# Optimization experiments

Measured on AMD Instinct MI355X. Metric: run time of the kernel, lower is better.

## Reference

```python
import jax, jax.numpy as jnp
import numpy as np

N_WIRES = 12
DEPTH = 4
IN_DIM = 256
BATCH = 4096


def _apply_rx(state, theta, wire, n):
    """Apply RX(theta) = [[cos(t/2), -i sin(t/2)], [-i sin(t/2), cos(t/2)]] on `wire`.
    state: (batch, 2^n) complex. theta: scalar or (batch,) float."""
    half = theta * 0.5
    c = jnp.reshape(jnp.cos(half), (-1, 1, 1))  # broadcasts for scalar or per-batch
    s = jnp.reshape(jnp.sin(half), (-1, 1, 1))
    L, R = 2 ** wire, 2 ** (n - wire - 1)
    st = state.reshape(-1, L, 2, R)
    a0, a1 = st[:, :, 0], st[:, :, 1]
    b0 = c * a0 - 1j * s * a1
    b1 = -1j * s * a0 + c * a1
    return jnp.stack([b0, b1], axis=2).reshape(state.shape)


def _apply_cnot_adj(state, ctrl, n):
    """CNOT with control=ctrl, target=ctrl+1 (adjacent wires)."""
    L, R = 2 ** ctrl, 2 ** (n - ctrl - 2)
    st = state.reshape(-1, L, 2, 2, R)
    c0 = st[:, :, 0]
    c1 = st[:, :, 1, ::-1]  # flip target bit when control=1
    return jnp.stack([c0, c1], axis=2).reshape(state.shape)


def _pauli_z_signs(n):
    idx = np.arange(2 ** n)
    # wire 0 is the most-significant bit (torchquantum convention)
    bits = (idx[:, None] >> (n - 1 - np.arange(n))[None, :]) & 1
    return (1.0 - 2.0 * bits).astype(np.float32)  # (2^n, n)


def setup_inputs() -> dict:
    key = jax.random.key(0)
    k1, k2, k3 = jax.random.split(key, 3)
    x = jax.random.normal(k1, (BATCH, IN_DIM), dtype=jnp.float32)
    W = jax.random.normal(k2, (N_WIRES, IN_DIM), dtype=jnp.float32)
    params = jax.random.normal(k3, (DEPTH, N_WIRES, 1), dtype=jnp.float32)
    return {"x": x, "W": W, "params": params}


def reference(x, W, params):
    n = W.shape[0]
    depth = params.shape[0]
    batch = x.shape[0]
    angles = x @ W.T  # (batch, n) -- nn.Linear without bias
    state = jnp.zeros((batch, 2 ** n), dtype=jnp.complex64).at[:, 0].set(1.0)
    # data-encoding RX layer (per-batch angles)
    for w in range(n):
        state = _apply_rx(state, angles[:, w], w, n)
    # variational layers: RX(params) then CNOT ladder
    for d in range(depth):
        for w in range(n):
            state = _apply_rx(state, params[d, w, 0], w, n)
        for w in range(n - 1):
            state = _apply_cnot_adj(state, w, n)
    probs = jnp.real(state * jnp.conj(state))  # (batch, 2^n)
    signs = jnp.asarray(_pauli_z_signs(n))     # (2^n, n)
    return probs @ signs  # <Z_w> per wire, (batch, n)
```

## Files before the change

### kernel.cpp

```cpp
#include <hip/hip_runtime.h>
#include <math.h>

#define N_WIRES 12
#define DEPTH   4
#define NGATES  (DEPTH * N_WIRES)
#define IN_DIM  256
#define ROWS_PER_BLOCK 16
#define XSTRIDE 272
#define K_BLOCKS 16


struct ConstTab {
    unsigned m[NGATES];
    float    wt[N_WIRES][NGATES];
    unsigned sh[N_WIRES][3];
};
struct MeasTab {
    unsigned S[N_WIRES];
};

__global__ __launch_bounds__(256)
void consts_kernel(const float* __restrict__ params, float* __restrict__ ws,
                   ConstTab ct)
{
    __shared__ float acc[N_WIRES * 16];
    const int t = threadIdx.x;
    if (t < N_WIRES * 16) acc[t] = 0.f;
    __syncthreads();

    const unsigned k = blockIdx.x * 256u + (unsigned)t;

    float th[NGATES];
    #pragma unroll
    for (int g = 0; g < NGATES; ++g) th[g] = params[g];

    float P[N_WIRES];
    #pragma unroll
    for (int w = 0; w < N_WIRES; ++w) P[w] = 0.f;

    #pragma unroll
    for (int g = 0; g < NGATES; ++g) {
        unsigned par = (unsigned)(__popc(ct.m[g] & k) & 1);
        float sg = __int_as_float(__float_as_int(th[g]) ^ (int)(par << 31));
        #pragma unroll
        for (int w = 0; w < N_WIRES; ++w)
            P[w] = fmaf(sg, ct.wt[w][g], P[w]);
    }

    #pragma unroll
    for (int w = 0; w < N_WIRES; ++w) {
        float sn, cs;
        sincosf(P[w], &sn, &cs);
        unsigned kap =  ((k >> ct.sh[w][0]) & 1u)
                     | (((k >> ct.sh[w][1]) & 1u) << 1)
                     | (((k >> ct.sh[w][2]) & 1u) << 2);
        atomicAdd(&acc[w * 16 + kap], cs);
        atomicAdd(&acc[w * 16 + 8 + kap], sn);
    }
    __syncthreads();
    if (t < N_WIRES * 16)
        ws[blockIdx.x * (N_WIRES * 16) + t] = acc[t];
}

__global__ __launch_bounds__(256)
void batch_kernel(const float* __restrict__ x, const float* __restrict__ W,
                  const float* __restrict__ ws, float* __restrict__ out,
                  MeasTab mt)
{
    __shared__ float xl[ROWS_PER_BLOCK * XSTRIDE];
    __shared__ float wl[N_WIRES * IN_DIM];
    __shared__ float al[ROWS_PER_BLOCK * N_WIRES];
    __shared__ float cl[N_WIRES * 16];
    const int t = threadIdx.x;
    const int rowbase = blockIdx.x * ROWS_PER_BLOCK;

    const float4* x4 = (const float4*)(x + (size_t)rowbase * IN_DIM);
    #pragma unroll
    for (int j = 0; j < 4; ++j) {
        int f   = t + 256 * j;
        int row = f >> 6;
        int c4  = f & 63;
        float4 v = x4[f];
        *(float4*)&xl[row * XSTRIDE + c4 * 4] = v;
    }
    const float4* W4 = (const float4*)W;
    #pragma unroll
    for (int j = 0; j < 3; ++j) {
        int f = t + 256 * j;
        ((float4*)wl)[f] = W4[f];
    }
    if (t < N_WIRES * 16) {
        float v = 0.f;
        #pragma unroll
        for (int p = 0; p < K_BLOCKS; ++p) v += ws[p * (N_WIRES * 16) + t];
        cl[t] = v;
    }
    __syncthreads();

    const int r = t >> 4, p = t & 15;
    float partial[N_WIRES];
    #pragma unroll
    for (int w = 0; w < N_WIRES; ++w) partial[w] = 0.f;
    for (int i = 0; i < 16; ++i) {
        float xv = xl[r * XSTRIDE + i * 16 + p];
        #pragma unroll
        for (int w = 0; w < N_WIRES; ++w)
            partial[w] = fmaf(xv, wl[w * IN_DIM + i * 16 + p], partial[w]);
    }
    #pragma unroll
    for (int w = 0; w < N_WIRES; ++w) {
        float v = partial[w];
        v += __shfl_xor(v, 1, 16);
        v += __shfl_xor(v, 2, 16);
        v += __shfl_xor(v, 4, 16);
        v += __shfl_xor(v, 8, 16);
        partial[w] = v;
    }
    if (p < N_WIRES) al[r * N_WIRES + p] = partial[p];
    __syncthreads();

    if (t < ROWS_PER_BLOCK * N_WIRES) {
        const int r2 = t / N_WIRES;
        const int w  = t - r2 * N_WIRES;
        unsigned S = mt.S[w];
        int pos[3], nb = 0;
        for (int b = 0; b < N_WIRES; ++b) if ((S >> b) & 1) pos[nb++] = b;
        float a[3] = {0.f, 0.f, 0.f};
        for (int j = 0; j < nb; ++j) a[j] = al[r2 * N_WIRES + pos[j]];
        float o = 0.f;
        const int nk = 1 << nb;
        for (int kap = 0; kap < nk; ++kap) {
            float B = 0.f;
            for (int j = 0; j < nb; ++j)
                B += ((kap >> j) & 1) ? -a[j] : a[j];
            float sn, cs;
            __sincosf(B, &sn, &cs);
            o = fmaf(cs,  cl[w * 16 + kap],     o);
            o = fmaf(-sn, cl[w * 16 + 8 + kap], o);
        }
        out[(size_t)(rowbase + r2) * N_WIRES + w] = o * (1.f / 4096.f);
    }
}

static void gf2_mul(const unsigned* A, const unsigned* B, unsigned* C) {
    for (int i = 0; i < N_WIRES; ++i) {
        unsigned r = 0;
        for (int v = 0; v < N_WIRES; ++v)
            if ((A[i] >> v) & 1) r ^= B[v];
        C[i] = r;
    }
}
static int popc_host(unsigned v) { int c = 0; while (v) { c += v & 1; v >>= 1; } return c; }

extern "C" void kernel_launch(void* const* d_in, const int* in_sizes, int n_in,
                              void* d_out, int out_size, void* d_ws, size_t ws_size,
                              hipStream_t stream) {
    const float* x      = (const float*)d_in[0];
    const float* W      = (const float*)d_in[1];
    const float* params = (const float*)d_in[2];
    float* out          = (float*)d_out;
    float* wsf          = (float*)d_ws;

    unsigned L[N_WIRES], Linv[N_WIRES];
    for (int w = 0; w < N_WIRES; ++w) {
        L[w]    = (1u << (w + 1)) - 1u;
        Linv[w] = (w == 0) ? 1u : ((1u << w) | (1u << (w - 1)));
    }
    unsigned Mp[DEPTH + 1][N_WIRES], Mi[DEPTH + 1][N_WIRES];
    for (int w = 0; w < N_WIRES; ++w) { Mp[0][w] = 1u << w; Mi[0][w] = 1u << w; }
    for (int d = 1; d <= DEPTH; ++d) {
        gf2_mul(L, Mp[d - 1], Mp[d]);
        gf2_mul(Linv, Mi[d - 1], Mi[d]);
    }

    ConstTab ct;
    MeasTab  mt;
    for (int d = 0; d < DEPTH; ++d)
        for (int w = 0; w < N_WIRES; ++w) {
            unsigned m = 0;
            for (int u = 0; u < N_WIRES; ++u)
                if ((Mi[d][u] >> w) & 1) m |= (1u << u);
            ct.m[d * N_WIRES + w] = m;
        }
    for (int w = 0; w < N_WIRES; ++w) mt.S[w] = Mp[DEPTH][w];

    for (int w = 0; w < N_WIRES; ++w) {
        for (int g = 0; g < NGATES; ++g)
            ct.wt[w][g] = (popc_host(ct.m[g] & mt.S[w]) & 1) ? 1.f : 0.f;
        int nb = 0;
        for (int b = 0; b < N_WIRES; ++b)
            if ((mt.S[w] >> b) & 1) ct.sh[w][nb++] = (unsigned)b;
        for (; nb < 3; ++nb) ct.sh[w][nb] = 31u;
    }

    const int batch = in_sizes[0] / IN_DIM;

    hipLaunchKernelGGL(consts_kernel, dim3(K_BLOCKS), dim3(256), 0, stream,
                       params, wsf, ct);
    hipLaunchKernelGGL(batch_kernel, dim3(batch / ROWS_PER_BLOCK), dim3(256), 0, stream,
                       x, W, wsf, out, mt);
}
```

Baseline: 75.39 us.

## Fuse constant-table kernel into batch kernel with compile-time GF(2) tables

Removes the separate consts kernel and its workspace round-trip. Each of the 256 blocks now recomputes the per-wire cos/sin table itself, using compile-time GF(2) masks, 16 sub-enumerations per thread, and wavefront shuffle reductions before shared atomics. The global x and W loads are issued first so their latency overlaps that table computation. In exchange, every block repeats the 4096-basis-state table work and register pressure rises, and the tables are now hardcoded to this circuit shape.

```diff
diff --git a/kernel.cpp b/kernel.cpp
--- a/kernel.cpp
+++ b/kernel.cpp
@@ -3,109 +3,150 @@
 
 #define N_WIRES 12
 #define DEPTH   4
-#define NGATES  (DEPTH * N_WIRES)
+#define NGATES  48
 #define IN_DIM  256
 #define ROWS_PER_BLOCK 16
 #define XSTRIDE 272
-#define K_BLOCKS 16
 
-
-struct ConstTab {
-    unsigned m[NGATES];
-    float    wt[N_WIRES][NGATES];
-    unsigned sh[N_WIRES][3];
+struct Tabs {
+    unsigned gm[NGATES];
+    bool     rel[N_WIRES][NGATES];
+    unsigned chi[NGATES];
+    unsigned comp[N_WIRES];
 };
-struct MeasTab {
-    unsigned S[N_WIRES];
-};
+constexpr int cparity(unsigned v) { int c = 0; while (v) { c ^= (int)(v & 1u); v >>= 1; } return c; }
+constexpr Tabs make_tabs() {
+    Tabs tb{};
+    for (int g = 0; g < NGATES; ++g) {
+        int d = g / N_WIRES, w = g % N_WIRES;
+        unsigned m = 1u << w;
+        if ((d == 1 || d == 3) && w + 1 < N_WIRES) m |= 1u << (w + 1);
+        if ((d == 2 || d == 3) && w + 2 < N_WIRES) m |= 1u << (w + 2);
+        if (d == 3 && w + 3 < N_WIRES)             m |= 1u << (w + 3);
+        tb.gm[g] = m;
+        unsigned c = 0;
+        for (int i = 0; i < 16; ++i) c |= (unsigned)cparity(m & 0xFu & (unsigned)i) << i;
+        tb.chi[g] = c;
+    }
+    for (int w = 0; w < N_WIRES; ++w) {
+        unsigned S = (1u << w) | (w >= 4 ? (1u << (w - 4)) : 0u) | (w >= 8 ? (1u << (w - 8)) : 0u);
+        for (int g = 0; g < NGATES; ++g) tb.rel[w][g] = cparity(tb.gm[g] & S) != 0;
+        unsigned lc = (w < 4) ? 0u
+                    : (w < 8) ? (1u << (w - 4))
+                    : ((1u << (w - 8)) | ((w - 4 < 6) ? (1u << (w - 4)) : 0u));
+        tb.comp[w] = 0x3Fu & ~lc;
+    }
+    return tb;
+}
+constexpr Tabs TB = make_tabs();
 
 __global__ __launch_bounds__(256)
-void consts_kernel(const float* __restrict__ params, float* __restrict__ ws,
-                   ConstTab ct)
+void fused_kernel(const float* __restrict__ x, const float* __restrict__ W,
+                  const float* __restrict__ params, float* __restrict__ out)
 {
-    __shared__ float acc[N_WIRES * 16];
+    __shared__ float xl[ROWS_PER_BLOCK * XSTRIDE];
+    __shared__ float wl[N_WIRES * IN_DIM];
+    __shared__ float al[ROWS_PER_BLOCK * N_WIRES];
+    __shared__ float tab[N_WIRES * 16];
     const int t = threadIdx.x;
-    if (t < N_WIRES * 16) acc[t] = 0.f;
+    const int lane = t & 63;
+    const int rowbase = blockIdx.x * ROWS_PER_BLOCK;
+
+    if (t < N_WIRES * 16) tab[t] = 0.f;
+
+    const float4* x4 = (const float4*)(x + (size_t)rowbase * IN_DIM);
+    float4 xr[4];
+    #pragma unroll
+    for (int j = 0; j < 4; ++j) xr[j] = x4[t + 256 * j];
+    const float4* W4 = (const float4*)W;
+    float4 wr[3];
+    #pragma unroll
+    for (int j = 0; j < 3; ++j) wr[j] = W4[t + 256 * j];
+
     __syncthreads();
-
-    const unsigned k = blockIdx.x * 256u + (unsigned)t;
 
     float th[NGATES];
     #pragma unroll
-    for (int g = 0; g < NGATES; ++g) th[g] = params[g];
+    for (int g = 0; g < NGATES; ++g) {
+        unsigned hs = (unsigned)(__popc((TB.gm[g] >> 4) & (unsigned)t) & 1);
+        th[g] = __int_as_float(__float_as_int(params[g]) ^ (int)(hs << 31));
+    }
 
-    float P[N_WIRES];
+    float P0[N_WIRES];
     #pragma unroll
-    for (int w = 0; w < N_WIRES; ++w) P[w] = 0.f;
+    for (int w = 0; w < N_WIRES; ++w) {
+        float p = 0.f;
+        #pragma unroll
+        for (int g = 0; g < NGATES; ++g)
+            if (TB.rel[w][g] && (TB.gm[g] & 0xFu) == 0u) p += th[g];
+        P0[w] = p;
+    }
 
+    float ca[N_WIRES][2], sa[N_WIRES][2];
     #pragma unroll
-    for (int g = 0; g < NGATES; ++g) {
-        unsigned par = (unsigned)(__popc(ct.m[g] & k) & 1);
-        float sg = __int_as_float(__float_as_int(th[g]) ^ (int)(par << 31));
+    for (int w = 0; w < N_WIRES; ++w)
+        ca[w][0] = ca[w][1] = sa[w][0] = sa[w][1] = 0.f;
+    #pragma unroll
+    for (int i = 0; i < 16; ++i) {
         #pragma unroll
-        for (int w = 0; w < N_WIRES; ++w)
-            P[w] = fmaf(sg, ct.wt[w][g], P[w]);
+        for (int w = 0; w < N_WIRES; ++w) {
+            float p = P0[w];
+            #pragma unroll
+            for (int g = 0; g < NGATES; ++g) {
+                if (TB.rel[w][g] && (TB.gm[g] & 0xFu) != 0u) {
+                    if ((TB.chi[g] >> i) & 1u) p -= th[g]; else p += th[g];
+                }
+            }
+            float sn, cs;
+            __sincosf(p, &sn, &cs);
+            const int b = (i >> (w & 3)) & 1;
+            ca[w][b] += cs; sa[w][b] += sn;
+        }
     }
 
     #pragma unroll
     for (int w = 0; w < N_WIRES; ++w) {
-        float sn, cs;
-        sincosf(P[w], &sn, &cs);
-        unsigned kap =  ((k >> ct.sh[w][0]) & 1u)
-                     | (((k >> ct.sh[w][1]) & 1u) << 1)
-                     | (((k >> ct.sh[w][2]) & 1u) << 2);
-        atomicAdd(&acc[w * 16 + kap], cs);
-        atomicAdd(&acc[w * 16 + 8 + kap], sn);
+        const unsigned comp = TB.comp[w];
+        float v0c = ca[w][0], v1c = ca[w][1], v0s = sa[w][0], v1s = sa[w][1];
+        #pragma unroll
+        for (int d = 0; d < 6; ++d) {
+            if (comp & (1u << d)) {
+                v0c += __shfl_xor(v0c, 1 << d, 64);
+                v1c += __shfl_xor(v1c, 1 << d, 64);
+                v0s += __shfl_xor(v0s, 1 << d, 64);
+                v1s += __shfl_xor(v1s, 1 << d, 64);
+            }
+        }
+        if ((unsigned)(lane & (int)comp) == 0u) {
+            unsigned fk = 0;
+            if (w >= 4 && w < 8) fk = ((unsigned)t >> (w - 4)) & 1u;
+            if (w >= 8) fk = (((unsigned)t >> (w - 8)) & 1u)
+                           | ((((unsigned)t >> (w - 4)) & 1u) << 1);
+            atomicAdd(&tab[w * 16 + (int)(fk << 1)],         v0c);
+            atomicAdd(&tab[w * 16 + (int)(fk << 1) + 1],     v1c);
+            atomicAdd(&tab[w * 16 + 8 + (int)(fk << 1)],     v0s);
+            atomicAdd(&tab[w * 16 + 8 + (int)(fk << 1) + 1], v1s);
+        }
     }
-    __syncthreads();
-    if (t < N_WIRES * 16)
-        ws[blockIdx.x * (N_WIRES * 16) + t] = acc[t];
-}
 
-__global__ __launch_bounds__(256)
-void batch_kernel(const float* __restrict__ x, const float* __restrict__ W,
-                  const float* __restrict__ ws, float* __restrict__ out,
-                  MeasTab mt)
-{
-    __shared__ float xl[ROWS_PER_BLOCK * XSTRIDE];
-    __shared__ float wl[N_WIRES * IN_DIM];
-    __shared__ float al[ROWS_PER_BLOCK * N_WIRES];
-    __shared__ float cl[N_WIRES * 16];
-    const int t = threadIdx.x;
-    const int rowbase = blockIdx.x * ROWS_PER_BLOCK;
-
-    const float4* x4 = (const float4*)(x + (size_t)rowbase * IN_DIM);
     #pragma unroll
     for (int j = 0; j < 4; ++j) {
-        int f   = t + 256 * j;
-        int row = f >> 6;
-        int c4  = f & 63;
-        float4 v = x4[f];
-        *(float4*)&xl[row * XSTRIDE + c4 * 4] = v;
+        int f = t + 256 * j, row = f >> 6, c4 = f & 63;
+        *(float4*)&xl[row * XSTRIDE + c4 * 4] = xr[j];
     }
-    const float4* W4 = (const float4*)W;
     #pragma unroll
-    for (int j = 0; j < 3; ++j) {
-        int f = t + 256 * j;
-        ((float4*)wl)[f] = W4[f];
-    }
-    if (t < N_WIRES * 16) {
-        float v = 0.f;
-        #pragma unroll
-        for (int p = 0; p < K_BLOCKS; ++p) v += ws[p * (N_WIRES * 16) + t];
-        cl[t] = v;
-    }
+    for (int j = 0; j < 3; ++j) ((float4*)wl)[t + 256 * j] = wr[j];
     __syncthreads();
 
     const int r = t >> 4, p = t & 15;
     float partial[N_WIRES];
     #pragma unroll
     for (int w = 0; w < N_WIRES; ++w) partial[w] = 0.f;
-    for (int i = 0; i < 16; ++i) {
-        float xv = xl[r * XSTRIDE + i * 16 + p];
+    for (int i2 = 0; i2 < 16; ++i2) {
+        float xv = xl[r * XSTRIDE + i2 * 16 + p];
         #pragma unroll
         for (int w = 0; w < N_WIRES; ++w)
-            partial[w] = fmaf(xv, wl[w * IN_DIM + i * 16 + p], partial[w]);
+            partial[w] = fmaf(xv, wl[w * IN_DIM + i2 * 16 + p], partial[w]);
     }
     #pragma unroll
     for (int w = 0; w < N_WIRES; ++w) {
@@ -122,35 +163,24 @@
     if (t < ROWS_PER_BLOCK * N_WIRES) {
         const int r2 = t / N_WIRES;
         const int w  = t - r2 * N_WIRES;
-        unsigned S = mt.S[w];
-        int pos[3], nb = 0;
-        for (int b = 0; b < N_WIRES; ++b) if ((S >> b) & 1) pos[nb++] = b;
-        float a[3] = {0.f, 0.f, 0.f};
-        for (int j = 0; j < nb; ++j) a[j] = al[r2 * N_WIRES + pos[j]];
+        const int nb = 1 + (w >= 4) + (w >= 8);
+        const float a0 = al[r2 * N_WIRES + (w & 3)];
+        const float a1 = (w >= 4) ? al[r2 * N_WIRES + ((w >= 8) ? (w - 4) : w)] : 0.f;
+        const float a2 = (w >= 8) ? al[r2 * N_WIRES + w] : 0.f;
         float o = 0.f;
         const int nk = 1 << nb;
         for (int kap = 0; kap < nk; ++kap) {
-            float B = 0.f;
-            for (int j = 0; j < nb; ++j)
-                B += ((kap >> j) & 1) ? -a[j] : a[j];
+            float B = (kap & 1) ? -a0 : a0;
+            if (nb > 1) B += (kap & 2) ? -a1 : a1;
+            if (nb > 2) B += (kap & 4) ? -a2 : a2;
             float sn, cs;
             __sincosf(B, &sn, &cs);
-            o = fmaf(cs,  cl[w * 16 + kap],     o);
-            o = fmaf(-sn, cl[w * 16 + 8 + kap], o);
+            o = fmaf(cs,  tab[w * 16 + kap],     o);
+            o = fmaf(-sn, tab[w * 16 + 8 + kap], o);
         }
         out[(size_t)(rowbase + r2) * N_WIRES + w] = o * (1.f / 4096.f);
     }
 }
-
-static void gf2_mul(const unsigned* A, const unsigned* B, unsigned* C) {
-    for (int i = 0; i < N_WIRES; ++i) {
-        unsigned r = 0;
-        for (int v = 0; v < N_WIRES; ++v)
-            if ((A[i] >> v) & 1) r ^= B[v];
-        C[i] = r;
-    }
-}
-static int popc_host(unsigned v) { int c = 0; while (v) { c += v & 1; v >>= 1; } return c; }
 
 extern "C" void kernel_launch(void* const* d_in, const int* in_sizes, int n_in,
                               void* d_out, int out_size, void* d_ws, size_t ws_size,
@@ -159,44 +189,9 @@
     const float* W      = (const float*)d_in[1];
     const float* params = (const float*)d_in[2];
     float* out          = (float*)d_out;
-    float* wsf          = (float*)d_ws;
-
-    unsigned L[N_WIRES], Linv[N_WIRES];
-    for (int w = 0; w < N_WIRES; ++w) {
-        L[w]    = (1u << (w + 1)) - 1u;
-        Linv[w] = (w == 0) ? 1u : ((1u << w) | (1u << (w - 1)));
-    }
-    unsigned Mp[DEPTH + 1][N_WIRES], Mi[DEPTH + 1][N_WIRES];
-    for (int w = 0; w < N_WIRES; ++w) { Mp[0][w] = 1u << w; Mi[0][w] = 1u << w; }
-    for (int d = 1; d <= DEPTH; ++d) {
-        gf2_mul(L, Mp[d - 1], Mp[d]);
-        gf2_mul(Linv, Mi[d - 1], Mi[d]);
-    }
-
-    ConstTab ct;
-    MeasTab  mt;
-    for (int d = 0; d < DEPTH; ++d)
-        for (int w = 0; w < N_WIRES; ++w) {
-            unsigned m = 0;
-            for (int u = 0; u < N_WIRES; ++u)
-                if ((Mi[d][u] >> w) & 1) m |= (1u << u);
-            ct.m[d * N_WIRES + w] = m;
-        }
-    for (int w = 0; w < N_WIRES; ++w) mt.S[w] = Mp[DEPTH][w];
-
-    for (int w = 0; w < N_WIRES; ++w) {
-        for (int g = 0; g < NGATES; ++g)
-            ct.wt[w][g] = (popc_host(ct.m[g] & mt.S[w]) & 1) ? 1.f : 0.f;
-        int nb = 0;
-        for (int b = 0; b < N_WIRES; ++b)
-            if ((mt.S[w] >> b) & 1) ct.sh[w][nb++] = (unsigned)b;
-        for (; nb < 3; ++nb) ct.sh[w][nb] = 31u;
-    }
+    (void)d_ws; (void)ws_size;
 
     const int batch = in_sizes[0] / IN_DIM;
-
-    hipLaunchKernelGGL(consts_kernel, dim3(K_BLOCKS), dim3(256), 0, stream,
-                       params, wsf, ct);
-    hipLaunchKernelGGL(batch_kernel, dim3(batch / ROWS_PER_BLOCK), dim3(256), 0, stream,
-                       x, W, wsf, out, mt);
+    hipLaunchKernelGGL(fused_kernel, dim3(batch / ROWS_PER_BLOCK), dim3(256), 0, stream,
+                       x, W, params, out);
 }
```

Result: faster. 70.70 us (-6.2%).
